# Kernel optimization log

Hardware: AMD Instinct MI355X
Metric: run time of the kernel (lower is better)

## Reference

```python
import jax, jax.numpy as jnp
import numpy as np
from jax.ops import segment_sum

N_NODES = 100000

def setup_inputs() -> dict:
    key = jax.random.key(0)
    k1, k2, k3 = jax.random.split(key, 3)
    x = jax.random.normal(k1, (N_NODES, 128), dtype=jnp.float32)
    edge_weight = jax.random.uniform(k2, (3200000,), dtype=jnp.float32)
    edge_index = jax.random.randint(k3, (2, 3200000), 0, N_NODES, dtype=jnp.int64)
    return {"x": x, "edge_weight": edge_weight, "edge_index": edge_index}

def reference(x, edge_weight, edge_index):
    # GCNConv with weight forced to identity (in==out channels, no bias):
    # lin(x) == x, so the op is gcn_norm + scatter-add aggregation.
    n = x.shape[0]
    # add self loops with fill value 1.0 (improved=False)
    loop_idx = jnp.arange(n, dtype=edge_index.dtype)
    row = jnp.concatenate([edge_index[0], loop_idx])
    col = jnp.concatenate([edge_index[1], loop_idx])
    ew = jnp.concatenate([edge_weight, jnp.ones((n,), dtype=edge_weight.dtype)])
    # symmetric normalization: deg computed at target (col)
    deg = segment_sum(ew, col, num_segments=n)
    dinv = jnp.where(deg > 0, jax.lax.rsqrt(deg), 0.0)
    norm = dinv[row] * ew * dinv[col]
    # message = norm * x[src]; aggregate (sum) at target
    msgs = x[row] * norm[:, None]          # [E+N, d]
    out = segment_sum(msgs, col, num_segments=n)  # [N, d]
    return out
```

## Files before the change

### kernel.cpp

```cpp
#include <hip/hip_runtime.h>
#include <hip/hip_fp16.h>
#include <math.h>

#define FEAT      128
#define PITCH     72
#define CH        6144
#define K_EDGES   12
#define MAXBINS   512
#define CAP_MAX   9216
#define K2        18

__global__ void conv_xs_kernel(const float* __restrict__ x,
                               const float* __restrict__ dinv,
                               __half2* __restrict__ xs, int n4) {
    int i = blockIdx.x * blockDim.x + threadIdx.x;
    if (i >= n4) return;
    float s = dinv[i >> 5];
    float4 v = ((const float4*)x)[i];
    xs[2 * i]     = __floats2half2_rn(s * v.x, s * v.y);
    xs[2 * i + 1] = __floats2half2_rn(s * v.z, s * v.w);
}

__global__ __launch_bounds__(512) void p1_partition_kernel(
        const int* __restrict__ row,
        const int* __restrict__ col,
        const float* __restrict__ ew,
        int* __restrict__ bin_cursor,
        unsigned long long* __restrict__ binned,
        int E, int NBINS, int cap) {
    __shared__ unsigned long long stage[CH];
    __shared__ int hist[MAXBINS];
    __shared__ int lofs[MAXBINS];
    __shared__ int lcnt[MAXBINS];
    __shared__ int gbase[MAXBINS];
    __shared__ int scanbuf[MAXBINS];
    int tid = threadIdx.x;
    if (tid < MAXBINS) { hist[tid] = 0; lcnt[tid] = 0; }
    __syncthreads();

    int start = blockIdx.x * CH;
    int end   = start + CH; if (end > E) end = E;
    int total = end - start;

    unsigned long long ed[K_EDGES];
    int ebin[K_EDGES];
    #pragma unroll
    for (int k = 0; k < K_EDGES; k++) {
        int e = start + (k << 9) + tid;
        if (e < end) {
            int c = col[e];
            unsigned short wh = __half_as_ushort(__float2half_rn(ew[e]));
            ed[k] = ((unsigned long long)wh << 48)
                  | ((unsigned long long)((unsigned)row[e] & 0xFFFFFFu) << 24)
                  | (unsigned)(c & 0xFFFFFFu);
            ebin[k] = c >> 8;
            atomicAdd(&hist[ebin[k]], 1);
        } else {
            ebin[k] = -1;
        }
    }
    __syncthreads();

    int h = (tid < NBINS) ? hist[tid] : 0;
    scanbuf[tid] = h;
    __syncthreads();
    #pragma unroll
    for (int off = 1; off < MAXBINS; off <<= 1) {
        int t = (tid >= off) ? scanbuf[tid - off] : 0;
        __syncthreads();
        scanbuf[tid] += t;
        __syncthreads();
    }
    lofs[tid] = scanbuf[tid] - h;
    __syncthreads();

    #pragma unroll
    for (int k = 0; k < K_EDGES; k++) {
        if (ebin[k] >= 0) {
            int pos = lofs[ebin[k]] + atomicAdd(&lcnt[ebin[k]], 1);
            stage[pos] = ed[k];
        }
    }
    if (tid < NBINS)
        gbase[tid] = hist[tid] ? atomicAdd(&bin_cursor[tid], hist[tid]) : 0;
    __syncthreads();

    for (int i = tid; i < total; i += 512) {
        unsigned long long e = stage[i];
        int bin = (int)((e >> 8) & 0xFFFFu);
        int pos = gbase[bin] + (i - lofs[bin]);
        if (pos < cap) binned[(size_t)bin * cap + pos] = e;
    }
}

__global__ __launch_bounds__(512) void p2_build_kernel(
        const unsigned long long* __restrict__ binned,
        const int* __restrict__ bin_cursor,
        unsigned long long* __restrict__ csr,
        float* __restrict__ dinv,
        int* __restrict__ countg,
        const float* __restrict__ x,
        __half2* __restrict__ xs,
        int N, int NBINS, int cap) {
    __shared__ float degf[256];
    __shared__ int cnt[256];
    __shared__ int pfx[256];
    __shared__ int lcnt[256];
    __shared__ float sdi[256];
    __shared__ int wsum[4];
    int tid = threadIdx.x;
    if (tid < 256) { degf[tid] = 0.0f; cnt[tid] = 0; lcnt[tid] = 0; }
    __syncthreads();

    int b = blockIdx.x;
    int nE = bin_cursor[b]; if (nE > cap) nE = cap;
    const unsigned long long* src = binned + (size_t)b * cap;
    int nodeBase = b << 8;

    for (int i = tid; i < nE; i += 512) {
        unsigned long long p = src[i];
        int cl = (int)(p & 255u);
        float w = __half2float(__ushort_as_half((unsigned short)(p >> 48)));
        atomicAdd(&cnt[cl], 1);
        atomicAdd(&degf[cl], w);
    }
    __syncthreads();

    if (tid < 256) {
        int w = tid >> 6, l = tid & 63;
        int v = cnt[tid];
        int inc = v;
        #pragma unroll
        for (int d = 1; d < 64; d <<= 1) {
            int t = __shfl_up(inc, d);
            if (l >= d) inc += t;
        }
        if (l == 63) wsum[w] = inc;
        pfx[tid] = inc - v;
    }
    __syncthreads();
    if (tid < 256) {
        int w = tid >> 6;
        int add = 0;
        for (int q = 0; q < w; q++) add += wsum[q];
        int p = pfx[tid] + add;
        pfx[tid] = p;
        int node = nodeBase + tid;
        if (node < N) {
            float di = rsqrtf(1.0f + degf[tid]);
            sdi[tid] = di;
            dinv[node] = di;
            int c2 = cnt[tid]; if (c2 > 255) c2 = 255;
            countg[node] = (int)((((unsigned)(b * cap + p)) << 8) | (unsigned)c2);
        } else {
            sdi[tid] = 0.0f;
        }
    }
    __syncthreads();

    size_t base = (size_t)b * cap;
    for (int i = tid; i < nE; i += 512) {
        unsigned long long p = src[i];
        int cl     = (int)(p & 255u);
        unsigned r = (unsigned)((p >> 24) & 0xFFFFFFu);
        float w = __half2float(__ushort_as_half((unsigned short)(p >> 48)));
        int slot = atomicAdd(&lcnt[cl], 1);
        csr[base + pfx[cl] + slot] =
            ((unsigned long long)__float_as_uint(w) << 32) | r;
    }

    int nValid = N - nodeBase; if (nValid > 256) nValid = 256;
    if (nValid > 0) {
        int total4 = nValid << 5;
        for (int idx = tid; idx < total4; idx += 512) {
            int cl = idx >> 5;
            float s = sdi[cl];
            size_t g = ((size_t)(nodeBase + cl) << 5) + (idx & 31);
            float4 v = ((const float4*)x)[g];
            xs[2 * g]     = __floats2half2_rn(s * v.x, s * v.y);
            xs[2 * g + 1] = __floats2half2_rn(s * v.z, s * v.w);
        }
    }
}

#define GLD(q)  unsigned long long p##q = eb[wid][j + q];               \
                unsigned r##q = (unsigned)p##q;                          \
                float w##q = __uint_as_float((unsigned)(p##q >> 32));    \
                __half2 h##q = xs[(r##q << 6) | lane];
#define GFMA(q, acc)  { float2 v##q = __half22float2(h##q);              \
                acc.x = fmaf(w##q, v##q.x, acc.x);                       \
                acc.y = fmaf(w##q, v##q.y, acc.y); }

__global__ __launch_bounds__(256) void gather_xs_kernel(
        const __half2* __restrict__ xs,
        const float* __restrict__ dinv,
        const int* __restrict__ countg,
        const unsigned long long* __restrict__ csr,
        float* __restrict__ out, int nodeBase, int nEnd) {
    __shared__ unsigned long long eb[4][64];
    int wid  = threadIdx.x >> 6;
    int node = nodeBase + blockIdx.x * 4 + wid;
    int lane = threadIdx.x & 63;
    if (node >= nEnd) return;

    float di = dinv[node];
    unsigned c = (unsigned)countg[node];
    int cnt = (int)(c & 255u);
    const unsigned long long* b = csr + (c >> 8);

    unsigned long long e0 = (lane < cnt) ? b[lane] : 0ULL;
    eb[wid][lane] = e0;

    unsigned xbase = ((unsigned)node << 6) | (unsigned)lane;
    float2 xv = __half22float2(xs[xbase]);
    float2 a0 = xv;
    float2 a1 = {0.f, 0.f}, a2 = {0.f, 0.f}, a3 = {0.f, 0.f};

    int m = cnt < 64 ? cnt : 64;
    int j = 0;
    for (; j + 16 <= m; j += 16) {
        GLD(0)  GLD(1)  GLD(2)  GLD(3)  GLD(4)  GLD(5)  GLD(6)  GLD(7)
        GLD(8)  GLD(9)  GLD(10) GLD(11) GLD(12) GLD(13) GLD(14) GLD(15)
        GFMA(0, a0)  GFMA(1, a1)  GFMA(2, a2)  GFMA(3, a3)
        GFMA(4, a0)  GFMA(5, a1)  GFMA(6, a2)  GFMA(7, a3)
        GFMA(8, a0)  GFMA(9, a1)  GFMA(10, a2) GFMA(11, a3)
        GFMA(12, a0) GFMA(13, a1) GFMA(14, a2) GFMA(15, a3)
    }
    for (; j + 8 <= m; j += 8) {
        GLD(0)  GLD(1)  GLD(2)  GLD(3)  GLD(4)  GLD(5)  GLD(6)  GLD(7)
        GFMA(0, a0)  GFMA(1, a1)  GFMA(2, a2)  GFMA(3, a3)
        GFMA(4, a0)  GFMA(5, a1)  GFMA(6, a2)  GFMA(7, a3)
    }
    for (; j + 4 <= m; j += 4) {
        GLD(0)  GLD(1)  GLD(2)  GLD(3)
        GFMA(0, a0)  GFMA(1, a1)  GFMA(2, a2)  GFMA(3, a3)
    }
    for (; j < m; ++j) {
        GLD(0)
        GFMA(0, a0)
    }
    for (; j < cnt; ++j) {
        unsigned long long p0 = b[j];
        unsigned r0 = (unsigned)p0;
        float w0 = __uint_as_float((unsigned)(p0 >> 32));
        float2 v0 = __half22float2(xs[(r0 << 6) | lane]);
        a0.x = fmaf(w0, v0.x, a0.x);  a0.y = fmaf(w0, v0.y, a0.y);
    }
    float2 r;
    r.x = di * ((a0.x + a1.x) + (a2.x + a3.x));
    r.y = di * ((a0.y + a1.y) + (a2.y + a3.y));
    ((float2*)(out + (size_t)node * FEAT))[lane] = r;
}


__global__ void init_packed_kernel(unsigned long long* __restrict__ packed, int n) {
    int i = blockIdx.x * blockDim.x + threadIdx.x;
    if (i < n) packed[i] = (1ULL << 32);
}

__global__ void passA_kernel(const int* __restrict__ row,
                             const int* __restrict__ col,
                             const float* __restrict__ ew,
                             unsigned long long* __restrict__ packed,
                             unsigned long long* __restrict__ bucket, int E) {
    int e = blockIdx.x * blockDim.x + threadIdx.x;
    if (e >= E) return;
    int c = col[e], r = row[e];
    float w = ew[e];
    unsigned long long v = (1ULL << 40)
        | (unsigned long long)((double)w * 4294967296.0);
    unsigned long long old = atomicAdd(&packed[c], v);
    unsigned int slot = (unsigned int)(old >> 40);
    if (slot < PITCH)
        bucket[(size_t)c * PITCH + slot] =
            ((unsigned long long)__float_as_uint(w) << 32) | ((unsigned int)r & 0xFFFFFFu);
}

__global__ void make_dinv_count_kernel(const unsigned long long* __restrict__ packed,
                                       float* __restrict__ dinv,
                                       int* __restrict__ countg, int n) {
    int i = blockIdx.x * blockDim.x + threadIdx.x;
    if (i < n) {
        unsigned long long p = packed[i];
        unsigned long long frac = p & ((1ULL << 40) - 1);
        float d = (float)((double)frac * (1.0 / 4294967296.0));
        dinv[i] = rsqrtf(d);
        int c = (int)(p >> 40); if (c > PITCH) c = PITCH;
        countg[i] = (int)((((unsigned)i * (unsigned)PITCH) << 8) | (unsigned)c);
    }
}


__global__ void init_deg_kernel(float* __restrict__ deg, int n) {
    int i = blockIdx.x * blockDim.x + threadIdx.x;
    if (i < n) deg[i] = 1.0f;
}
__global__ void deg_accum_kernel(const int* __restrict__ col,
                                 const float* __restrict__ ew,
                                 float* __restrict__ deg, int E) {
    int e = blockIdx.x * blockDim.x + threadIdx.x;
    if (e < E) atomicAdd(&deg[col[e]], ew[e]);
}
__global__ void make_dinv_kernel(const float* __restrict__ deg,
                                 float* __restrict__ dinv, int n) {
    int i = blockIdx.x * blockDim.x + threadIdx.x;
    if (i < n) {
        float d = deg[i];
        dinv[i] = d > 0.0f ? rsqrtf(d) : 0.0f;
    }
}
__global__ void init_out_kernel(const float* __restrict__ x,
                                const float* __restrict__ dinv,
                                float* __restrict__ out, int n) {
    int idx = blockIdx.x * blockDim.x + threadIdx.x;
    int i = idx >> 5, lane = idx & 31;
    if (i >= n) return;
    float s = dinv[i] * dinv[i];
    float4 v = ((const float4*)(x + (size_t)i * FEAT))[lane];
    float4 r;
    r.x = s * v.x; r.y = s * v.y; r.z = s * v.z; r.w = s * v.w;
    ((float4*)(out + (size_t)i * FEAT))[lane] = r;
}
__global__ void scatter_kernel(const float* __restrict__ x,
                               const float* __restrict__ ew,
                               const int* __restrict__ row,
                               const int* __restrict__ col,
                               const float* __restrict__ dinv,
                               float* __restrict__ out, int E) {
    long long idx = (long long)blockIdx.x * blockDim.x + threadIdx.x;
    int e = (int)(idx >> 5), lane = (int)(idx & 31);
    if (e >= E) return;
    int r = row[e], c = col[e];
    float nrm = dinv[r] * ew[e] * dinv[c];
    float4 v = ((const float4*)(x + (size_t)r * FEAT))[lane];
    float* o = out + (size_t)c * FEAT + lane * 4;
    atomicAdd(o + 0, nrm * v.x);
    atomicAdd(o + 1, nrm * v.y);
    atomicAdd(o + 2, nrm * v.z);
    atomicAdd(o + 3, nrm * v.w);
}


static inline size_t align256(size_t v) { return (v + 255) & ~(size_t)255; }

extern "C" void kernel_launch(void* const* d_in, const int* in_sizes, int n_in,
                              void* d_out, int out_size, void* d_ws, size_t ws_size,
                              hipStream_t stream) {
    const float* x  = (const float*)d_in[0];
    const float* ew = (const float*)d_in[1];
    const int*   ei = (const int*)d_in[2];

    const int N = in_sizes[0] / FEAT;
    const int E = in_sizes[1];
    const int* row = ei;
    const int* col = ei + E;

    float* out = (float*)d_out;
    const int B = 256;
    char* w = (char*)d_ws;

    const int NBINS = (N + 255) >> 8;
    const int avg   = (E + NBINS - 1) / NBINS;
    int cap = avg + 8 * (int)sqrt((double)avg) + 64;
    if (cap > CAP_MAX) cap = CAP_MAX;

    size_t sz_bucket = align256((size_t)N * PITCH * 8);
    size_t sz_dinv   = align256((size_t)N * 4);
    size_t sz_count  = align256((size_t)N * 4);
    size_t sz_cursor = align256((size_t)NBINS * 4);
    size_t sz_binned = align256((size_t)NBINS * (size_t)cap * 8);
    size_t sz_xs     = align256((size_t)N * FEAT * 2);

    size_t need_fast2 = sz_binned  + sz_dinv + sz_count + sz_cursor
                      + sz_binned + sz_xs;
    size_t need_fast1 = align256((size_t)N * 8) + sz_dinv + sz_count + sz_xs + sz_bucket;

    int n4 = N * FEAT / 4;

    if (ws_size >= need_fast2 && NBINS <= MAXBINS && N < (1 << 24) && E < (1 << 24)) {
        unsigned long long* csr = (unsigned long long*)w;     w += sz_binned;
        float* dinv   = (float*)w;                            w += sz_dinv;
        int*   countg = (int*)w;                              w += sz_count;
        int*   cursor = (int*)w;                              w += sz_cursor;
        unsigned long long* binned = (unsigned long long*)w;  w += sz_binned;
        __half2* xs = (__half2*)w;

        hipMemsetAsync(cursor, 0, (size_t)NBINS * 4, stream);
        int p1b = (E + CH - 1) / CH;
        p1_partition_kernel<<<p1b, 512, 0, stream>>>(row, col, ew, cursor, binned,
                                                     E, NBINS, cap);
        p2_build_kernel<<<NBINS, 512, 0, stream>>>(binned, cursor, csr,
                                                   dinv, countg, x, xs, N, NBINS, cap);
        gather_xs_kernel<<<(N + 3) / 4, B, 0, stream>>>(xs, dinv, countg, csr,
                                                        out, 0, N);
    } else if (ws_size >= need_fast1 && N < (1 << 24) &&
               (size_t)N * PITCH < (size_t)(1 << 24)) {
        unsigned long long* packed = (unsigned long long*)w;  w += align256((size_t)N * 8);
        float*   dinv   = (float*)w;                          w += sz_dinv;
        int*     countg = (int*)w;                            w += sz_count;
        __half2* xs     = (__half2*)w;                        w += sz_xs;
        unsigned long long* bucket = (unsigned long long*)w;

        init_packed_kernel<<<(N + B - 1) / B, B, 0, stream>>>(packed, N);
        passA_kernel<<<(E + B - 1) / B, B, 0, stream>>>(row, col, ew, packed, bucket, E);
        make_dinv_count_kernel<<<(N + B - 1) / B, B, 0, stream>>>(packed, dinv, countg, N);
        conv_xs_kernel<<<(n4 + B - 1) / B, B, 0, stream>>>(x, dinv, xs, n4);
        gather_xs_kernel<<<(N + 3) / 4, B, 0, stream>>>(xs, dinv, countg, bucket, out, 0, N);
    } else {
        float* deg  = (float*)w;                  w += sz_dinv;
        float* dinv = (float*)w;
        init_deg_kernel<<<(N + B - 1) / B, B, 0, stream>>>(deg, N);
        deg_accum_kernel<<<(E + B - 1) / B, B, 0, stream>>>(col, ew, deg, E);
        make_dinv_kernel<<<(N + B - 1) / B, B, 0, stream>>>(deg, dinv, N);
        long long it = (long long)N * 32;
        init_out_kernel<<<(int)((it + B - 1) / B), B, 0, stream>>>(x, dinv, out, N);
        long long st = (long long)E * 32;
        scatter_kernel<<<(int)((st + B - 1) / B), B, 0, stream>>>(x, ew, row, col, dinv, out, E);
    }
}
```

Baseline: 315.5 us.

## Split CSR build into half-bin blocks with LDS staging and compact CSR

The CSR build kernel now launches two blocks per 256-node bin. Each block handles 128 nodes, stages its edges in shared memory and writes them contiguously to a compact CSR region claimed through a global atomic cursor. The point is to double parallelism in the build phase and replace scattered global writes with coalesced ones. The gather kernel also switches to nontemporal loads for edge lists and nontemporal stores for output. Each half-block still scans the whole bin, so global reads in that phase double. A new guard falls back to another path when a half-bin could overflow the shared stage buffer.

```diff
diff --git a/kernel.cpp b/kernel.cpp
--- a/kernel.cpp
+++ b/kernel.cpp
@@ -8,7 +8,7 @@
 #define K_EDGES   12
 #define MAXBINS   512
 #define CAP_MAX   9216
-#define K2        18
+#define STAGE2    4768
 
 __global__ void conv_xs_kernel(const float* __restrict__ x,
                                const float* __restrict__ dinv,
@@ -95,38 +95,44 @@
 
 __global__ __launch_bounds__(512) void p2_build_kernel(
         const unsigned long long* __restrict__ binned,
-        const int* __restrict__ bin_cursor,
+        int* __restrict__ bin_cursor,
         unsigned long long* __restrict__ csr,
         float* __restrict__ dinv,
         int* __restrict__ countg,
         const float* __restrict__ x,
         __half2* __restrict__ xs,
         int N, int NBINS, int cap) {
-    __shared__ float degf[256];
-    __shared__ int cnt[256];
-    __shared__ int pfx[256];
-    __shared__ int lcnt[256];
-    __shared__ float sdi[256];
-    __shared__ int wsum[4];
+    __shared__ unsigned long long stage[STAGE2];
+    __shared__ float degf[128];
+    __shared__ int cnt[128];
+    __shared__ int pfx[128];
+    __shared__ int lcnt[128];
+    __shared__ float sdi[128];
+    __shared__ int wsum[2];
+    __shared__ int binBase_s;
     int tid = threadIdx.x;
-    if (tid < 256) { degf[tid] = 0.0f; cnt[tid] = 0; lcnt[tid] = 0; }
-    __syncthreads();
-
-    int b = blockIdx.x;
+    if (tid < 128) { degf[tid] = 0.0f; cnt[tid] = 0; lcnt[tid] = 0; }
+    __syncthreads();
+
+    int b  = blockIdx.x >> 1;
+    int hf = blockIdx.x & 1;
     int nE = bin_cursor[b]; if (nE > cap) nE = cap;
     const unsigned long long* src = binned + (size_t)b * cap;
-    int nodeBase = b << 8;
+    int nodeBase = (b << 8) | (hf << 7);
 
     for (int i = tid; i < nE; i += 512) {
         unsigned long long p = src[i];
         int cl = (int)(p & 255u);
-        float w = __half2float(__ushort_as_half((unsigned short)(p >> 48)));
-        atomicAdd(&cnt[cl], 1);
-        atomicAdd(&degf[cl], w);
-    }
-    __syncthreads();
-
-    if (tid < 256) {
+        if ((cl >> 7) == hf) {
+            int cl1 = cl & 127;
+            float w = __half2float(__ushort_as_half((unsigned short)(p >> 48)));
+            atomicAdd(&cnt[cl1], 1);
+            atomicAdd(&degf[cl1], w);
+        }
+    }
+    __syncthreads();
+
+    if (tid < 128) {
         int w = tid >> 6, l = tid & 63;
         int v = cnt[tid];
         int inc = v;
@@ -139,37 +145,47 @@
         pfx[tid] = inc - v;
     }
     __syncthreads();
-    if (tid < 256) {
-        int w = tid >> 6;
-        int add = 0;
-        for (int q = 0; q < w; q++) add += wsum[q];
-        int p = pfx[tid] + add;
-        pfx[tid] = p;
+    if (tid < 128 && tid >= 64) pfx[tid] += wsum[0];
+    __syncthreads();
+    if (tid == 0) binBase_s = atomicAdd(&bin_cursor[NBINS], pfx[127] + cnt[127]);
+    __syncthreads();
+
+    int binBase = binBase_s;
+    if (tid < 128) {
         int node = nodeBase + tid;
         if (node < N) {
             float di = rsqrtf(1.0f + degf[tid]);
             sdi[tid] = di;
             dinv[node] = di;
             int c2 = cnt[tid]; if (c2 > 255) c2 = 255;
-            countg[node] = (int)((((unsigned)(b * cap + p)) << 8) | (unsigned)c2);
+            countg[node] = (int)((((unsigned)(binBase + pfx[tid])) << 8) | (unsigned)c2);
         } else {
             sdi[tid] = 0.0f;
         }
     }
-    __syncthreads();
-
-    size_t base = (size_t)b * cap;
+
     for (int i = tid; i < nE; i += 512) {
         unsigned long long p = src[i];
-        int cl     = (int)(p & 255u);
-        unsigned r = (unsigned)((p >> 24) & 0xFFFFFFu);
-        float w = __half2float(__ushort_as_half((unsigned short)(p >> 48)));
-        int slot = atomicAdd(&lcnt[cl], 1);
-        csr[base + pfx[cl] + slot] =
-            ((unsigned long long)__float_as_uint(w) << 32) | r;
-    }
-
-    int nValid = N - nodeBase; if (nValid > 256) nValid = 256;
+        int cl = (int)(p & 255u);
+        if ((cl >> 7) == hf) {
+            int cl1 = cl & 127;
+            unsigned r = (unsigned)((p >> 24) & 0xFFFFFFu);
+            float w = __half2float(__ushort_as_half((unsigned short)(p >> 48)));
+            int slot = atomicAdd(&lcnt[cl1], 1);
+            int pos = pfx[cl1] + slot;
+            if (pos < STAGE2)
+                stage[pos] = ((unsigned long long)__float_as_uint(w) << 32) | r;
+        }
+    }
+    __syncthreads();
+
+    int totalE = pfx[127] + cnt[127];
+    if (totalE > STAGE2) totalE = STAGE2;
+    for (int i = tid; i < totalE; i += 512)
+        csr[(size_t)binBase + i] = stage[i];
+
+    int nValid = N - nodeBase;
+    if (nValid > 128) nValid = 128;
     if (nValid > 0) {
         int total4 = nValid << 5;
         for (int idx = tid; idx < total4; idx += 512) {
@@ -208,7 +224,7 @@
     int cnt = (int)(c & 255u);
     const unsigned long long* b = csr + (c >> 8);
 
-    unsigned long long e0 = (lane < cnt) ? b[lane] : 0ULL;
+    unsigned long long e0 = (lane < cnt) ? __builtin_nontemporal_load(b + lane) : 0ULL;
     eb[wid][lane] = e0;
 
     unsigned xbase = ((unsigned)node << 6) | (unsigned)lane;
@@ -240,7 +256,7 @@
         GFMA(0, a0)
     }
     for (; j < cnt; ++j) {
-        unsigned long long p0 = b[j];
+        unsigned long long p0 = __builtin_nontemporal_load(b + j);
         unsigned r0 = (unsigned)p0;
         float w0 = __uint_as_float((unsigned)(p0 >> 32));
         float2 v0 = __half22float2(xs[(r0 << 6) | lane]);
@@ -249,7 +265,10 @@
     float2 r;
     r.x = di * ((a0.x + a1.x) + (a2.x + a3.x));
     r.y = di * ((a0.y + a1.y) + (a2.y + a3.y));
-    ((float2*)(out + (size_t)node * FEAT))[lane] = r;
+    unsigned long long rv;
+    __builtin_memcpy(&rv, &r, 8);
+    __builtin_nontemporal_store(rv,
+        (unsigned long long*)(out + (size_t)node * FEAT) + lane);
 }
 
 
@@ -364,33 +383,37 @@
     int cap = avg + 8 * (int)sqrt((double)avg) + 64;
     if (cap > CAP_MAX) cap = CAP_MAX;
 
+    size_t sz_csr    = align256((size_t)E * 8 + 256);
     size_t sz_bucket = align256((size_t)N * PITCH * 8);
     size_t sz_dinv   = align256((size_t)N * 4);
     size_t sz_count  = align256((size_t)N * 4);
-    size_t sz_cursor = align256((size_t)NBINS * 4);
+    size_t sz_cursor = align256((size_t)(NBINS + 1) * 4);
     size_t sz_binned = align256((size_t)NBINS * (size_t)cap * 8);
     size_t sz_xs     = align256((size_t)N * FEAT * 2);
 
-    size_t need_fast2 = sz_binned  + sz_dinv + sz_count + sz_cursor
-                      + sz_binned + sz_xs;
+    size_t need_fast2 = sz_csr + sz_dinv + sz_count + sz_cursor + sz_binned + sz_xs;
     size_t need_fast1 = align256((size_t)N * 8) + sz_dinv + sz_count + sz_xs + sz_bucket;
 
     int n4 = N * FEAT / 4;
 
-    if (ws_size >= need_fast2 && NBINS <= MAXBINS && N < (1 << 24) && E < (1 << 24)) {
-        unsigned long long* csr = (unsigned long long*)w;     w += sz_binned;
+    bool half_ok = (avg / 2 + 6 * (int)sqrt((double)avg) + 64) <= STAGE2;
+
+    if (ws_size >= need_fast2 && NBINS <= MAXBINS && N < (1 << 24) && E < (1 << 24)
+        && half_ok) {
+        unsigned long long* csr = (unsigned long long*)w;     w += sz_csr;
         float* dinv   = (float*)w;                            w += sz_dinv;
         int*   countg = (int*)w;                              w += sz_count;
         int*   cursor = (int*)w;                              w += sz_cursor;
         unsigned long long* binned = (unsigned long long*)w;  w += sz_binned;
         __half2* xs = (__half2*)w;
 
-        hipMemsetAsync(cursor, 0, (size_t)NBINS * 4, stream);
+        hipMemsetAsync(cursor, 0, (size_t)(NBINS + 1) * 4, stream);
         int p1b = (E + CH - 1) / CH;
         p1_partition_kernel<<<p1b, 512, 0, stream>>>(row, col, ew, cursor, binned,
                                                      E, NBINS, cap);
-        p2_build_kernel<<<NBINS, 512, 0, stream>>>(binned, cursor, csr,
-                                                   dinv, countg, x, xs, N, NBINS, cap);
+        p2_build_kernel<<<2 * NBINS, 512, 0, stream>>>(binned, cursor, csr,
+                                                       dinv, countg, x, xs,
+                                                       N, NBINS, cap);
         gather_xs_kernel<<<(N + 3) / 4, B, 0, stream>>>(xs, dinv, countg, csr,
                                                         out, 0, N);
     } else if (ws_size >= need_fast1 && N < (1 << 24) &&
```

After: 298.3 us. -5.4%, faster.
